# Kernel optimization log

Hardware: AMD Instinct MI355X
Metric: run time of the kernel (lower is better)

The kernel has to match this reference:

```python
import jax, jax.numpy as jnp
import numpy as np

B, C, Hh, Ww = 64, 128, 28, 28   # batch, channels, subband H, subband W (H/2, W/2 of input)
NB, BS = 4, 32                    # num_blocks, block_size (C = NB*BS)
ORI = 6                           # DTCWT orientation subbands


def setup_inputs() -> dict:
    key = jax.random.key(0)
    ks = jax.random.split(key, 7)
    return {
        "xl": jax.random.normal(ks[0], (B, C, Hh, Ww), jnp.float32),
        "xh": jax.random.normal(ks[1], (B, C, ORI, Hh, Ww, 2), jnp.float32),
        "w_ll": jax.random.normal(ks[2], (C, Hh, Ww), jnp.float32) * 0.02,
        "w1": jax.random.normal(ks[3], (2, NB, BS, BS), jnp.float32) * 0.02,
        "w2": jax.random.normal(ks[4], (2, NB, BS, BS), jnp.float32) * 0.02,
        "b1": jax.random.normal(ks[5], (2, NB, BS), jnp.float32) * 0.02,
        "b2": jax.random.normal(ks[6], (2, NB, BS), jnp.float32) * 0.02,
    }


def _mul(x, w):
    # block-diagonal matmul: x [..., nb, bs_in], w [nb, bs_in, bs_out]
    return jnp.einsum('...bd,bdk->...bk', x, w)


def reference(xl, xh, w_ll, w1, w2, b1, b2):
    # lowpass: elementwise weighting (broadcast over batch)
    xl_out = xl * w_ll

    b, c = xh.shape[0], xh.shape[1]
    # (B,C,6,H,W,2) -> (2,B,6,H,W,C) -> (2,B,6,H,W,NB,BS)
    x = jnp.transpose(xh, (5, 0, 2, 3, 4, 1))
    x = x.reshape(2, b, ORI, xh.shape[3], xh.shape[4], NB, BS)
    xr, xi = x[0], x[1]

    # complex block-diagonal layer 1 + ReLU
    r1 = jax.nn.relu(_mul(xr, w1[0]) - _mul(xi, w1[1]) + b1[0])
    i1 = jax.nn.relu(_mul(xr, w1[1]) + _mul(xi, w1[0]) + b1[1])
    # complex block-diagonal layer 2 (linear)
    r2 = _mul(r1, w2[0]) - _mul(i1, w2[1]) + b2[0]
    i2 = _mul(r1, w2[1]) + _mul(i1, w2[0]) + b2[1]

    # stack real/imag last, merge blocks back to C, restore (B,C,6,H,W,2)
    out = jnp.stack([r2, i2], axis=-1)                               # (B,6,H,W,NB,BS,2)
    out = out.reshape(b, ORI, xh.shape[3], xh.shape[4], NB * BS, 2)  # (B,6,H,W,C,2)
    xh_out = jnp.transpose(out, (0, 4, 1, 2, 3, 5))                  # (B,C,6,H,W,2)
    # softshrink lambd == 0.0 -> identity (the torch code skips it)
    return xl_out, xh_out
```

## Files before the change

### kernel.cpp

```cpp
#include <hip/hip_runtime.h>

typedef __bf16 bf16x8 __attribute__((ext_vector_type(8)));
typedef float  f32x4  __attribute__((ext_vector_type(4)));


static __device__ __forceinline__ unsigned short bf16bits(float f) {
  __bf16 h = (__bf16)f; return __builtin_bit_cast(unsigned short, h);
}
static __device__ __forceinline__ unsigned int pack2(float a, float b) {
  return (unsigned int)bf16bits(a) | ((unsigned int)bf16bits(b) << 16);
}

__global__ void prep_weights(const float* __restrict__ w1, const float* __restrict__ w2,
                             unsigned short* __restrict__ wg) {
  const int e = blockIdx.x * 256 + threadIdx.x;
  const int nb    = e >> 13;
  const int layer = (e >> 12) & 1;
  const int n = (e >> 6) & 63;
  const int k = e & 63;
  const float* w = layer ? w2 : w1;
  const int kk = k & 31, nn = n & 31;
  float v;
  if (n < 32) {
    v = (k < 32) ?  w[((0 * 4 + nb) * 32 + kk) * 32 + nn]
                 : -w[((1 * 4 + nb) * 32 + kk) * 32 + nn];
  } else {
    v = (k < 32) ?  w[((1 * 4 + nb) * 32 + kk) * 32 + nn]
                 :  w[((0 * 4 + nb) * 32 + kk) * 32 + nn];
  }
  const int pos = nb * 8192 + layer * 4096 + n * 64 + (((k >> 3) ^ ((n >> 1) & 7)) * 8) + (k & 7);
  wg[pos] = bf16bits(v);
}

__global__ __launch_bounds__(256, 3)
void fused_kernel(const float* __restrict__ xh, const unsigned short* __restrict__ wg,
                  const float* __restrict__ b1, const float* __restrict__ b2,
                  const float* __restrict__ xl, const float* __restrict__ wll,
                  float* __restrict__ out) {
  __shared__ __align__(16) unsigned short Xs[256 * 64];
  __shared__ __align__(16) unsigned short Ws[2 * 64 * 64];
  __shared__ __align__(16) float Bs[128];

  const int t = threadIdx.x;
  const int bi = blockIdx.x;

  if ((bi & 3) == 3) {
    const int llb = bi >> 2;
    const float4* xi4 = reinterpret_cast<const float4*>(xl);
    const float4* w4  = reinterpret_cast<const float4*>(wll);
    float4* o4 = reinterpret_cast<float4*>(out);
#pragma unroll
    for (int j = 0; j < 4; ++j) {
      const int i = llb * 1024 + j * 256 + t;
      const float4 x = xi4[i];
      const float4 w = w4[i % 25088];
      float4 r; r.x = x.x * w.x; r.y = x.y * w.y; r.z = x.z * w.z; r.w = x.w * w.w;
      o4[i] = r;
    }
    return;
  }

  const int xi = (bi >> 2) * 3 + (bi & 3);
  const int mt  = xi % 196;
  const int snb = xi / 196;
  const int ori = snb >> 2;
  const int nb  = snb & 3;
  const int p0 = mt << 8;

  char* XB = reinterpret_cast<char*>(Xs);
  const char* WB = reinterpret_cast<const char*>(Ws);
  const float* xb = xh + (size_t)(nb * 32) * 9408 + ori * 1568;
  float* ob = out + 6422528 + (size_t)(nb * 32) * 9408 + ori * 1568;

  f32x4 R[16];
  uint4 Wr[4];
  float Bv = 0.f;

  const int lr16 = t & 15;
  const int cg   = (t >> 4) & 3;
  const int wvi  = t >> 6;
#pragma unroll
  for (int j = 0; j < 8; ++j) {
    const int c = 2 * cg + 8 * (j >> 1);
    const int p = 2 * lr16 + 32 * (wvi * 2 + (j & 1));
    const int P = p0 + p;
    const int bb = P / 784;
    const int hw = P - bb * 784;
    const float* s = xb + (size_t)bb * 1204224 + c * 9408 + hw * 2;
    R[2 * j]     = *reinterpret_cast<const f32x4*>(s);
    R[2 * j + 1] = *reinterpret_cast<const f32x4*>(s + 9408);
  }
  {
    const uint4* src = reinterpret_cast<const uint4*>(wg + nb * 8192);
#pragma unroll
    for (int it = 0; it < 4; ++it) Wr[it] = src[it * 256 + t];
  }
  if (t < 128) {
    const int layer = t >> 6, n = t & 63;
    const float* bsrc = layer ? b2 : b1;
    Bv = bsrc[((n >> 5) * 4 + nb) * 32 + (n & 31)];
  }
  __builtin_amdgcn_sched_barrier(0);

  {
    uint4* dst = reinterpret_cast<uint4*>(Ws);
#pragma unroll
    for (int it = 0; it < 4; ++it) dst[it * 256 + t] = Wr[it];
  }
  if (t < 128) Bs[t] = Bv;
#pragma unroll
  for (int j = 0; j < 8; ++j) {
    const int c = 2 * cg + 8 * (j >> 1);
    const int p = 2 * lr16 + 32 * (wvi * 2 + (j & 1));
    const int g0 = c >> 3;
    const int off = (c & 7) * 2;
    const int s0 = (p >> 1) & 7;
    const f32x4 vA = R[2 * j], vB = R[2 * j + 1];
    *reinterpret_cast<unsigned int*>(XB + p * 128 + ((g0 ^ s0) * 16) + off)             = pack2(vA[0], vB[0]);
    *reinterpret_cast<unsigned int*>(XB + p * 128 + (((g0 + 4) ^ s0) * 16) + off)       = pack2(vA[1], vB[1]);
    *reinterpret_cast<unsigned int*>(XB + (p + 1) * 128 + ((g0 ^ s0) * 16) + off)       = pack2(vA[2], vB[2]);
    *reinterpret_cast<unsigned int*>(XB + (p + 1) * 128 + (((g0 + 4) ^ s0) * 16) + off) = pack2(vA[3], vB[3]);
  }
  __syncthreads();

  const int lane = t & 63;
  const int wv = t >> 6;
  const int lr = lane & 15;
  const int lg = lane >> 4;

  f32x4 acc[4][4];
#pragma unroll
  for (int mi = 0; mi < 4; ++mi)
#pragma unroll
    for (int ni = 0; ni < 4; ++ni)
      acc[mi][ni] = (f32x4){0.f, 0.f, 0.f, 0.f};

#pragma unroll
  for (int ks = 0; ks < 2; ++ks) {
    bf16x8 wf[4], xf[4];
#pragma unroll
    for (int mi = 0; mi < 4; ++mi) {
      const int n = mi * 16 + lr;
      wf[mi] = *reinterpret_cast<const bf16x8*>(WB + n * 128 + (((ks * 4 + lg) ^ ((n >> 1) & 7)) * 16));
    }
#pragma unroll
    for (int ni = 0; ni < 4; ++ni) {
      const int p = wv * 64 + ni * 16 + lr;
      xf[ni] = *reinterpret_cast<const bf16x8*>(XB + p * 128 + (((ks * 4 + lg) ^ ((p >> 1) & 7)) * 16));
    }
#pragma unroll
    for (int mi = 0; mi < 4; ++mi)
#pragma unroll
      for (int ni = 0; ni < 4; ++ni)
        acc[mi][ni] = __builtin_amdgcn_mfma_f32_16x16x32_bf16(wf[mi], xf[ni], acc[mi][ni], 0, 0, 0);
  }

#pragma unroll
  for (int mi = 0; mi < 4; ++mi) {
    const f32x4 bv = *reinterpret_cast<const f32x4*>(&Bs[mi * 16 + lg * 4]);
    const int gH = mi * 2 + (lg >> 1);
    const int offH = (lg & 1) * 8;
#pragma unroll
    for (int ni = 0; ni < 4; ++ni) {
      const int p = wv * 64 + ni * 16 + lr;
      const float h0 = fmaxf(acc[mi][ni][0] + bv[0], 0.f);
      const float h1 = fmaxf(acc[mi][ni][1] + bv[1], 0.f);
      const float h2 = fmaxf(acc[mi][ni][2] + bv[2], 0.f);
      const float h3 = fmaxf(acc[mi][ni][3] + bv[3], 0.f);
      uint2 u; u.x = pack2(h0, h1); u.y = pack2(h2, h3);
      *reinterpret_cast<uint2*>(XB + p * 128 + ((gH ^ ((p >> 1) & 7)) * 16) + offH) = u;
    }
  }

  f32x4 acc2[4][4];
#pragma unroll
  for (int mi = 0; mi < 4; ++mi)
#pragma unroll
    for (int ni = 0; ni < 4; ++ni)
      acc2[mi][ni] = (f32x4){0.f, 0.f, 0.f, 0.f};

#pragma unroll
  for (int ks = 0; ks < 2; ++ks) {
    bf16x8 wf[4], hf[4];
#pragma unroll
    for (int mi = 0; mi < 4; ++mi) {
      const int n = mi * 16 + lr;
      wf[mi] = *reinterpret_cast<const bf16x8*>(WB + 8192 + n * 128 + (((ks * 4 + lg) ^ ((n >> 1) & 7)) * 16));
    }
#pragma unroll
    for (int ni = 0; ni < 4; ++ni) {
      const int p = wv * 64 + ni * 16 + lr;
      hf[ni] = *reinterpret_cast<const bf16x8*>(XB + p * 128 + (((ks * 4 + lg) ^ ((p >> 1) & 7)) * 16));
    }
#pragma unroll
    for (int mi = 0; mi < 4; ++mi)
#pragma unroll
      for (int ni = 0; ni < 4; ++ni)
        acc2[mi][ni] = __builtin_amdgcn_mfma_f32_16x16x32_bf16(wf[mi], hf[ni], acc2[mi][ni], 0, 0, 0);
  }

#pragma unroll
  for (int ni = 0; ni < 4; ++ni) {
    const int p = wv * 64 + ni * 16 + lr;
    const int P = p0 + p;
    const int bb = P / 784;
    const int hw = P - bb * 784;
    float* obase = ob + (size_t)bb * 1204224 + hw * 2;
#pragma unroll
    for (int mi = 0; mi < 2; ++mi) {
      const f32x4 bre = *reinterpret_cast<const f32x4*>(&Bs[64 + mi * 16 + lg * 4]);
      const f32x4 bim = *reinterpret_cast<const f32x4*>(&Bs[64 + (mi + 2) * 16 + lg * 4]);
#pragma unroll
      for (int j = 0; j < 4; ++j) {
        const int c = mi * 16 + lg * 4 + j;
        float2 v;
        v.x = acc2[mi][ni][j] + bre[j];
        v.y = acc2[mi + 2][ni][j] + bim[j];
        *reinterpret_cast<float2*>(obase + (size_t)c * 9408) = v;
      }
    }
  }
}

extern "C" void kernel_launch(void* const* d_in, const int* in_sizes, int n_in,
                              void* d_out, int out_size, void* d_ws, size_t ws_size,
                              hipStream_t stream) {
  (void)in_sizes; (void)n_in; (void)out_size; (void)ws_size;
  const float* xl  = (const float*)d_in[0];
  const float* xh  = (const float*)d_in[1];
  const float* wll = (const float*)d_in[2];
  const float* w1  = (const float*)d_in[3];
  const float* w2  = (const float*)d_in[4];
  const float* b1  = (const float*)d_in[5];
  const float* b2  = (const float*)d_in[6];
  float* out = (float*)d_out;
  unsigned short* wg = (unsigned short*)d_ws;

  prep_weights<<<128, 256, 0, stream>>>(w1, w2, wg);
  fused_kernel<<<6272, 256, 0, stream>>>(xh, wg, b1, b2, xl, wll, out);
}
```

Before: 148.7 us.

## Process four tiles per block with register-prefetched next-tile loads

Each high-pass block now loops over four 256-pixel tiles instead of one. While the current tile is packed into LDS and run through both MFMA layers, the global loads for the next tile are already issued. Weights are copied to LDS and biases loaded into registers once per block, and the shared bias buffer is removed. The grid shrinks fourfold, and the low-pass blocks also handle four times more data with batched loads. This trades fewer blocks and lower occupancy (launch bounds 3 to 2) for latency hiding and amortised setup. Register pressure rises because the prefetch buffer stays live across the compute.

```diff
diff --git a/kernel.cpp b/kernel.cpp
--- a/kernel.cpp
+++ b/kernel.cpp
@@ -32,14 +32,13 @@
   wg[pos] = bf16bits(v);
 }
 
-__global__ __launch_bounds__(256, 3)
+__global__ __launch_bounds__(256, 2)
 void fused_kernel(const float* __restrict__ xh, const unsigned short* __restrict__ wg,
                   const float* __restrict__ b1, const float* __restrict__ b2,
                   const float* __restrict__ xl, const float* __restrict__ wll,
                   float* __restrict__ out) {
   __shared__ __align__(16) unsigned short Xs[256 * 64];
   __shared__ __align__(16) unsigned short Ws[2 * 64 * 64];
-  __shared__ __align__(16) float Bs[128];
 
   const int t = threadIdx.x;
   const int bi = blockIdx.x;
@@ -50,22 +49,38 @@
     const float4* w4  = reinterpret_cast<const float4*>(wll);
     float4* o4 = reinterpret_cast<float4*>(out);
 #pragma unroll
-    for (int j = 0; j < 4; ++j) {
-      const int i = llb * 1024 + j * 256 + t;
-      const float4 x = xi4[i];
-      const float4 w = w4[i % 25088];
-      float4 r; r.x = x.x * w.x; r.y = x.y * w.y; r.z = x.z * w.z; r.w = x.w * w.w;
-      o4[i] = r;
+    for (int jj = 0; jj < 4; ++jj) {
+      float4 x[4], w[4];
+#pragma unroll
+      for (int j = 0; j < 4; ++j) {
+        const int i = llb * 4096 + (jj * 4 + j) * 256 + t;
+        x[j] = xi4[i];
+        w[j] = w4[i % 25088];
+      }
+#pragma unroll
+      for (int j = 0; j < 4; ++j) {
+        const int i = llb * 4096 + (jj * 4 + j) * 256 + t;
+        float4 r; r.x = x[j].x * w[j].x; r.y = x[j].y * w[j].y;
+        r.z = x[j].z * w[j].z; r.w = x[j].w * w[j].w;
+        o4[i] = r;
+      }
     }
     return;
   }
 
   const int xi = (bi >> 2) * 3 + (bi & 3);
-  const int mt  = xi % 196;
-  const int snb = xi / 196;
+  const int tg  = xi % 49;
+  const int snb = xi / 49;
   const int ori = snb >> 2;
   const int nb  = snb & 3;
-  const int p0 = mt << 8;
+  const int p00 = tg << 10;
+
+  const int lane = t & 63;
+  const int wv = t >> 6;
+  const int lr = lane & 15;
+  const int lg = lane >> 4;
+  const int lr16 = t & 15;
+  const int cg   = (t >> 4) & 3;
 
   char* XB = reinterpret_cast<char*>(Xs);
   const char* WB = reinterpret_cast<const char*>(Ws);
@@ -73,150 +88,150 @@
   float* ob = out + 6422528 + (size_t)(nb * 32) * 9408 + ori * 1568;
 
   f32x4 R[16];
-  uint4 Wr[4];
-  float Bv = 0.f;
-
-  const int lr16 = t & 15;
-  const int cg   = (t >> 4) & 3;
-  const int wvi  = t >> 6;
-#pragma unroll
-  for (int j = 0; j < 8; ++j) {
-    const int c = 2 * cg + 8 * (j >> 1);
-    const int p = 2 * lr16 + 32 * (wvi * 2 + (j & 1));
-    const int P = p0 + p;
-    const int bb = P / 784;
-    const int hw = P - bb * 784;
-    const float* s = xb + (size_t)bb * 1204224 + c * 9408 + hw * 2;
-    R[2 * j]     = *reinterpret_cast<const f32x4*>(s);
-    R[2 * j + 1] = *reinterpret_cast<const f32x4*>(s + 9408);
-  }
+
+  auto issueX = [&](int p0) {
+#pragma unroll
+    for (int j = 0; j < 8; ++j) {
+      const int c = 2 * cg + 8 * (j >> 1);
+      const int p = 2 * lr16 + 32 * (wv * 2 + (j & 1));
+      const int P = p0 + p;
+      const int bb = P / 784;
+      const int hw = P - bb * 784;
+      const float* s = xb + (size_t)bb * 1204224 + c * 9408 + hw * 2;
+      R[2 * j]     = *reinterpret_cast<const f32x4*>(s);
+      R[2 * j + 1] = *reinterpret_cast<const f32x4*>(s + 9408);
+    }
+  };
+  auto packX = [&]() {
+#pragma unroll
+    for (int j = 0; j < 8; ++j) {
+      const int c = 2 * cg + 8 * (j >> 1);
+      const int p = 2 * lr16 + 32 * (wv * 2 + (j & 1));
+      const int g0 = c >> 3;
+      const int off = (c & 7) * 2;
+      const int s0 = (p >> 1) & 7;
+      const f32x4 vA = R[2 * j], vB = R[2 * j + 1];
+      *reinterpret_cast<unsigned int*>(XB + p * 128 + ((g0 ^ s0) * 16) + off)             = pack2(vA[0], vB[0]);
+      *reinterpret_cast<unsigned int*>(XB + p * 128 + (((g0 + 4) ^ s0) * 16) + off)       = pack2(vA[1], vB[1]);
+      *reinterpret_cast<unsigned int*>(XB + (p + 1) * 128 + ((g0 ^ s0) * 16) + off)       = pack2(vA[2], vB[2]);
+      *reinterpret_cast<unsigned int*>(XB + (p + 1) * 128 + (((g0 + 4) ^ s0) * 16) + off) = pack2(vA[3], vB[3]);
+    }
+  };
+
+  issueX(p00);
   {
     const uint4* src = reinterpret_cast<const uint4*>(wg + nb * 8192);
-#pragma unroll
-    for (int it = 0; it < 4; ++it) Wr[it] = src[it * 256 + t];
-  }
-  if (t < 128) {
-    const int layer = t >> 6, n = t & 63;
-    const float* bsrc = layer ? b2 : b1;
-    Bv = bsrc[((n >> 5) * 4 + nb) * 32 + (n & 31)];
-  }
-  __builtin_amdgcn_sched_barrier(0);
-
-  {
     uint4* dst = reinterpret_cast<uint4*>(Ws);
 #pragma unroll
-    for (int it = 0; it < 4; ++it) dst[it * 256 + t] = Wr[it];
-  }
-  if (t < 128) Bs[t] = Bv;
-#pragma unroll
-  for (int j = 0; j < 8; ++j) {
-    const int c = 2 * cg + 8 * (j >> 1);
-    const int p = 2 * lr16 + 32 * (wvi * 2 + (j & 1));
-    const int g0 = c >> 3;
-    const int off = (c & 7) * 2;
-    const int s0 = (p >> 1) & 7;
-    const f32x4 vA = R[2 * j], vB = R[2 * j + 1];
-    *reinterpret_cast<unsigned int*>(XB + p * 128 + ((g0 ^ s0) * 16) + off)             = pack2(vA[0], vB[0]);
-    *reinterpret_cast<unsigned int*>(XB + p * 128 + (((g0 + 4) ^ s0) * 16) + off)       = pack2(vA[1], vB[1]);
-    *reinterpret_cast<unsigned int*>(XB + (p + 1) * 128 + ((g0 ^ s0) * 16) + off)       = pack2(vA[2], vB[2]);
-    *reinterpret_cast<unsigned int*>(XB + (p + 1) * 128 + (((g0 + 4) ^ s0) * 16) + off) = pack2(vA[3], vB[3]);
+    for (int it = 0; it < 4; ++it) dst[it * 256 + t] = src[it * 256 + t];
+  }
+  f32x4 bv1[4];
+#pragma unroll
+  for (int mi = 0; mi < 4; ++mi)
+    bv1[mi] = *reinterpret_cast<const f32x4*>(b1 + (mi >> 1) * 128 + nb * 32 + (mi & 1) * 16 + lg * 4);
+  f32x4 bre2[2], bim2[2];
+#pragma unroll
+  for (int mi = 0; mi < 2; ++mi) {
+    bre2[mi] = *reinterpret_cast<const f32x4*>(b2 + nb * 32 + mi * 16 + lg * 4);
+    bim2[mi] = *reinterpret_cast<const f32x4*>(b2 + 128 + nb * 32 + mi * 16 + lg * 4);
   }
   __syncthreads();
 
-  const int lane = t & 63;
-  const int wv = t >> 6;
-  const int lr = lane & 15;
-  const int lg = lane >> 4;
-
-  f32x4 acc[4][4];
-#pragma unroll
-  for (int mi = 0; mi < 4; ++mi)
-#pragma unroll
-    for (int ni = 0; ni < 4; ++ni)
-      acc[mi][ni] = (f32x4){0.f, 0.f, 0.f, 0.f};
-
-#pragma unroll
-  for (int ks = 0; ks < 2; ++ks) {
-    bf16x8 wf[4], xf[4];
+#pragma unroll
+  for (int tt = 0; tt < 4; ++tt) {
+    const int p0 = p00 + tt * 256;
+
+    packX();
+    if (tt < 3) issueX(p0 + 256);
+    __builtin_amdgcn_sched_barrier(0);
+
+    f32x4 acc[4][4];
+#pragma unroll
+    for (int mi = 0; mi < 4; ++mi)
+#pragma unroll
+      for (int ni = 0; ni < 4; ++ni)
+        acc[mi][ni] = (f32x4){0.f, 0.f, 0.f, 0.f};
+
+#pragma unroll
+    for (int ks = 0; ks < 2; ++ks) {
+      bf16x8 wf[4], xf[4];
+#pragma unroll
+      for (int mi = 0; mi < 4; ++mi) {
+        const int n = mi * 16 + lr;
+        wf[mi] = *reinterpret_cast<const bf16x8*>(WB + n * 128 + (((ks * 4 + lg) ^ ((n >> 1) & 7)) * 16));
+      }
+#pragma unroll
+      for (int ni = 0; ni < 4; ++ni) {
+        const int p = wv * 64 + ni * 16 + lr;
+        xf[ni] = *reinterpret_cast<const bf16x8*>(XB + p * 128 + (((ks * 4 + lg) ^ ((p >> 1) & 7)) * 16));
+      }
+#pragma unroll
+      for (int mi = 0; mi < 4; ++mi)
+#pragma unroll
+        for (int ni = 0; ni < 4; ++ni)
+          acc[mi][ni] = __builtin_amdgcn_mfma_f32_16x16x32_bf16(wf[mi], xf[ni], acc[mi][ni], 0, 0, 0);
+    }
+
 #pragma unroll
     for (int mi = 0; mi < 4; ++mi) {
-      const int n = mi * 16 + lr;
-      wf[mi] = *reinterpret_cast<const bf16x8*>(WB + n * 128 + (((ks * 4 + lg) ^ ((n >> 1) & 7)) * 16));
-    }
+      const int gH = mi * 2 + (lg >> 1);
+      const int offH = (lg & 1) * 8;
+#pragma unroll
+      for (int ni = 0; ni < 4; ++ni) {
+        const int p = wv * 64 + ni * 16 + lr;
+        const float h0 = fmaxf(acc[mi][ni][0] + bv1[mi][0], 0.f);
+        const float h1 = fmaxf(acc[mi][ni][1] + bv1[mi][1], 0.f);
+        const float h2 = fmaxf(acc[mi][ni][2] + bv1[mi][2], 0.f);
+        const float h3 = fmaxf(acc[mi][ni][3] + bv1[mi][3], 0.f);
+        uint2 u; u.x = pack2(h0, h1); u.y = pack2(h2, h3);
+        *reinterpret_cast<uint2*>(XB + p * 128 + ((gH ^ ((p >> 1) & 7)) * 16) + offH) = u;
+      }
+    }
+
+    f32x4 acc2[4][4];
+#pragma unroll
+    for (int mi = 0; mi < 4; ++mi)
+#pragma unroll
+      for (int ni = 0; ni < 4; ++ni)
+        acc2[mi][ni] = (f32x4){0.f, 0.f, 0.f, 0.f};
+
+#pragma unroll
+    for (int ks = 0; ks < 2; ++ks) {
+      bf16x8 wf[4], hf[4];
+#pragma unroll
+      for (int mi = 0; mi < 4; ++mi) {
+        const int n = mi * 16 + lr;
+        wf[mi] = *reinterpret_cast<const bf16x8*>(WB + 8192 + n * 128 + (((ks * 4 + lg) ^ ((n >> 1) & 7)) * 16));
+      }
+#pragma unroll
+      for (int ni = 0; ni < 4; ++ni) {
+        const int p = wv * 64 + ni * 16 + lr;
+        hf[ni] = *reinterpret_cast<const bf16x8*>(XB + p * 128 + (((ks * 4 + lg) ^ ((p >> 1) & 7)) * 16));
+      }
+#pragma unroll
+      for (int mi = 0; mi < 4; ++mi)
+#pragma unroll
+        for (int ni = 0; ni < 4; ++ni)
+          acc2[mi][ni] = __builtin_amdgcn_mfma_f32_16x16x32_bf16(wf[mi], hf[ni], acc2[mi][ni], 0, 0, 0);
+    }
+
 #pragma unroll
     for (int ni = 0; ni < 4; ++ni) {
       const int p = wv * 64 + ni * 16 + lr;
-      xf[ni] = *reinterpret_cast<const bf16x8*>(XB + p * 128 + (((ks * 4 + lg) ^ ((p >> 1) & 7)) * 16));
-    }
-#pragma unroll
-    for (int mi = 0; mi < 4; ++mi)
-#pragma unroll
-      for (int ni = 0; ni < 4; ++ni)
-        acc[mi][ni] = __builtin_amdgcn_mfma_f32_16x16x32_bf16(wf[mi], xf[ni], acc[mi][ni], 0, 0, 0);
-  }
-
-#pragma unroll
-  for (int mi = 0; mi < 4; ++mi) {
-    const f32x4 bv = *reinterpret_cast<const f32x4*>(&Bs[mi * 16 + lg * 4]);
-    const int gH = mi * 2 + (lg >> 1);
-    const int offH = (lg & 1) * 8;
-#pragma unroll
-    for (int ni = 0; ni < 4; ++ni) {
-      const int p = wv * 64 + ni * 16 + lr;
-      const float h0 = fmaxf(acc[mi][ni][0] + bv[0], 0.f);
-      const float h1 = fmaxf(acc[mi][ni][1] + bv[1], 0.f);
-      const float h2 = fmaxf(acc[mi][ni][2] + bv[2], 0.f);
-      const float h3 = fmaxf(acc[mi][ni][3] + bv[3], 0.f);
-      uint2 u; u.x = pack2(h0, h1); u.y = pack2(h2, h3);
-      *reinterpret_cast<uint2*>(XB + p * 128 + ((gH ^ ((p >> 1) & 7)) * 16) + offH) = u;
-    }
-  }
-
-  f32x4 acc2[4][4];
-#pragma unroll
-  for (int mi = 0; mi < 4; ++mi)
-#pragma unroll
-    for (int ni = 0; ni < 4; ++ni)
-      acc2[mi][ni] = (f32x4){0.f, 0.f, 0.f, 0.f};
-
-#pragma unroll
-  for (int ks = 0; ks < 2; ++ks) {
-    bf16x8 wf[4], hf[4];
-#pragma unroll
-    for (int mi = 0; mi < 4; ++mi) {
-      const int n = mi * 16 + lr;
-      wf[mi] = *reinterpret_cast<const bf16x8*>(WB + 8192 + n * 128 + (((ks * 4 + lg) ^ ((n >> 1) & 7)) * 16));
-    }
-#pragma unroll
-    for (int ni = 0; ni < 4; ++ni) {
-      const int p = wv * 64 + ni * 16 + lr;
-      hf[ni] = *reinterpret_cast<const bf16x8*>(XB + p * 128 + (((ks * 4 + lg) ^ ((p >> 1) & 7)) * 16));
-    }
-#pragma unroll
-    for (int mi = 0; mi < 4; ++mi)
-#pragma unroll
-      for (int ni = 0; ni < 4; ++ni)
-        acc2[mi][ni] = __builtin_amdgcn_mfma_f32_16x16x32_bf16(wf[mi], hf[ni], acc2[mi][ni], 0, 0, 0);
-  }
-
-#pragma unroll
-  for (int ni = 0; ni < 4; ++ni) {
-    const int p = wv * 64 + ni * 16 + lr;
-    const int P = p0 + p;
-    const int bb = P / 784;
-    const int hw = P - bb * 784;
-    float* obase = ob + (size_t)bb * 1204224 + hw * 2;
-#pragma unroll
-    for (int mi = 0; mi < 2; ++mi) {
-      const f32x4 bre = *reinterpret_cast<const f32x4*>(&Bs[64 + mi * 16 + lg * 4]);
-      const f32x4 bim = *reinterpret_cast<const f32x4*>(&Bs[64 + (mi + 2) * 16 + lg * 4]);
-#pragma unroll
-      for (int j = 0; j < 4; ++j) {
-        const int c = mi * 16 + lg * 4 + j;
-        float2 v;
-        v.x = acc2[mi][ni][j] + bre[j];
-        v.y = acc2[mi + 2][ni][j] + bim[j];
-        *reinterpret_cast<float2*>(obase + (size_t)c * 9408) = v;
+      const int P = p0 + p;
+      const int bb = P / 784;
+      const int hw = P - bb * 784;
+      float* obase = ob + (size_t)bb * 1204224 + hw * 2;
+#pragma unroll
+      for (int mi = 0; mi < 2; ++mi) {
+#pragma unroll
+        for (int j = 0; j < 4; ++j) {
+          const int c = mi * 16 + lg * 4 + j;
+          float2 v;
+          v.x = acc2[mi][ni][j] + bre2[mi][j];
+          v.y = acc2[mi + 2][ni][j] + bim2[mi][j];
+          *reinterpret_cast<float2*>(obase + (size_t)c * 9408) = v;
+        }
       }
     }
   }
@@ -237,5 +252,5 @@
   unsigned short* wg = (unsigned short*)d_ws;
 
   prep_weights<<<128, 256, 0, stream>>>(w1, w2, wg);
-  fused_kernel<<<6272, 256, 0, stream>>>(xh, wg, b1, b2, xl, wll, out);
-}
+  fused_kernel<<<1568, 256, 0, stream>>>(xh, wg, b1, b2, xl, wll, out);
+}
```

Measured after the change: 155.6 us. 1.05x slower.
